# Kernel optimization log

Hardware: AMD Instinct MI355X
Metric: run time of the kernel (lower is better)

The kernel has to match this reference:

```python
import jax, jax.numpy as jnp
import numpy as np

HID = 4096
NH = 64
HD = HID // NH            # 64
ROT = int(0.5 * HD)       # 32, partial rotary
THETA = 25000.0
EPS = 1e-5
NEG = jnp.finfo(jnp.float32).min


def setup_inputs() -> dict:
    key = jax.random.key(0)
    ks = jax.random.split(key, 8)
    B, S = 1, 2048
    hidden_states = jax.random.normal(ks[0], (B, S, HID), dtype=jnp.float32)
    # causal additive mask [B,1,S,S]
    causal = jnp.where(jnp.tril(jnp.ones((S, S), dtype=bool)), 0.0, NEG)
    attention_mask = jnp.broadcast_to(causal, (B, 1, S, S)).astype(jnp.float32)
    position_ids = jnp.broadcast_to(jnp.arange(S, dtype=jnp.int32), (B, S))
    sc = 1.0 / np.sqrt(HID)
    W_qkv = jax.random.normal(ks[1], (HID, 3 * HID), dtype=jnp.float32) * sc
    b_qkv = jnp.zeros((3 * HID,), dtype=jnp.float32)
    W_dense = jax.random.normal(ks[2], (HID, HID), dtype=jnp.float32) * sc
    b_dense = jnp.zeros((HID,), dtype=jnp.float32)
    q_ln_w = jnp.ones((HD,), dtype=jnp.float32)
    q_ln_b = jnp.zeros((HD,), dtype=jnp.float32)
    k_ln_w = jnp.ones((HD,), dtype=jnp.float32)
    k_ln_b = jnp.zeros((HD,), dtype=jnp.float32)
    return dict(hidden_states=hidden_states, attention_mask=attention_mask,
                position_ids=position_ids, W_qkv=W_qkv, b_qkv=b_qkv,
                W_dense=W_dense, b_dense=b_dense,
                q_ln_w=q_ln_w, q_ln_b=q_ln_b, k_ln_w=k_ln_w, k_ln_b=k_ln_b)


def _layernorm(x, w, b):
    mu = jnp.mean(x, axis=-1, keepdims=True)
    var = jnp.mean(jnp.square(x - mu), axis=-1, keepdims=True)
    return (x - mu) * jax.lax.rsqrt(var + EPS) * w + b


def _rope_cos_sin(seq_len, position_ids):
    inv_freq = 1.0 / (THETA ** (jnp.arange(0, ROT, 2, dtype=jnp.float32) / ROT))
    t = jnp.arange(seq_len, dtype=jnp.float32)
    freqs = jnp.einsum('s,f->sf', t, inv_freq)        # [S, ROT/2]
    emb = jnp.concatenate([freqs, freqs], axis=-1)    # [S, ROT]
    cos = jnp.cos(emb)[position_ids][:, None, :, :]   # [B,1,S,ROT]
    sin = jnp.sin(emb)[position_ids][:, None, :, :]
    return cos, sin


def _rotate_half(x):
    x1, x2 = jnp.split(x, 2, axis=-1)
    return jnp.concatenate([-x2, x1], axis=-1)


def reference(hidden_states, attention_mask, position_ids, W_qkv, b_qkv,
              W_dense, b_dense, q_ln_w, q_ln_b, k_ln_w, k_ln_b):
    B, S, _ = hidden_states.shape
    fused = hidden_states @ W_qkv + b_qkv                 # [B,S,3*HID]
    fused = fused.reshape(B, S, NH, 3, HD)
    q, k, v = fused[..., 0, :], fused[..., 1, :], fused[..., 2, :]  # [B,S,NH,HD]
    q = _layernorm(q, q_ln_w, q_ln_b)
    k = _layernorm(k, k_ln_w, k_ln_b)
    q = q.transpose(0, 2, 1, 3)                           # [B,NH,S,HD]
    k = k.transpose(0, 2, 1, 3)
    v = v.transpose(0, 2, 1, 3)
    cos, sin = _rope_cos_sin(S, position_ids)
    q_rot, q_pass = q[..., :ROT], q[..., ROT:]
    k_rot, k_pass = k[..., :ROT], k[..., ROT:]
    q_rot = q_rot * cos + _rotate_half(q_rot) * sin
    k_rot = k_rot * cos + _rotate_half(k_rot) * sin
    q = jnp.concatenate([q_rot, q_pass], axis=-1)
    k = jnp.concatenate([k_rot, k_pass], axis=-1)
    scores = jnp.einsum('bhqd,bhkd->bhqk', q, k) / np.sqrt(HD)
    scores = scores + attention_mask
    probs = jax.nn.softmax(scores.astype(jnp.float32), axis=-1).astype(q.dtype)
    attn = jnp.einsum('bhqk,bhkd->bhqd', probs, v)        # [B,NH,S,HD]
    attn = attn.transpose(0, 2, 1, 3).reshape(B, S, HID)
    return attn @ W_dense + b_dense
```

## Files before the change

### kernel.cpp

```cpp
#include <hip/hip_runtime.h>
#include <hip/hip_bf16.h>


typedef __attribute__((ext_vector_type(4))) unsigned int u32x4;
typedef __attribute__((ext_vector_type(8))) __bf16 bf16x8;
typedef __attribute__((ext_vector_type(4))) float f32x4;

__device__ __forceinline__ bf16x8 frag_ld(const __hip_bfloat16* p) {
  return __builtin_bit_cast(bf16x8, *(const u32x4*)p);
}

__device__ __forceinline__ void gll16(const __hip_bfloat16* g,
                                      __hip_bfloat16* l) {
  __builtin_amdgcn_global_load_lds(
      (const __attribute__((address_space(1))) unsigned int*)g,
      (__attribute__((address_space(3))) unsigned int*)l, 16, 0, 0);
}

__global__ __launch_bounds__(256) void cvt_kernel(
    const float* __restrict__ in, __hip_bfloat16* __restrict__ out, int n4) {
  int i = blockIdx.x * 256 + threadIdx.x;
  if (i < n4) {
    float4 v = ((const float4*)in)[i];
    union { __hip_bfloat16 h[4]; unsigned long long u; } pk;
    pk.h[0] = __float2bfloat16(v.x);
    pk.h[1] = __float2bfloat16(v.y);
    pk.h[2] = __float2bfloat16(v.z);
    pk.h[3] = __float2bfloat16(v.w);
    ((unsigned long long*)out)[i] = pk.u;
  }
}

__global__ __launch_bounds__(256) void transpose_kernel(
    const float* __restrict__ W, __hip_bfloat16* __restrict__ WT,
    int K, int ldW, int colStride, int colOff) {
  __shared__ __align__(16) __hip_bfloat16 tile[64 * 72];
  const int t = threadIdx.x;
  const int c0 = blockIdx.x * colStride + colOff;
  const int n0 = blockIdx.x * 64;
  const int k0 = blockIdx.y * 64;
  for (int c = t; c < 1024; c += 256) {
    int row = c >> 4, col4 = (c & 15) << 2;
    float4 v = *(const float4*)&W[(size_t)(k0 + row) * ldW + c0 + col4];
    union { __hip_bfloat16 h[4]; unsigned long long u; } pk;
    pk.h[0] = __float2bfloat16(v.x);
    pk.h[1] = __float2bfloat16(v.y);
    pk.h[2] = __float2bfloat16(v.z);
    pk.h[3] = __float2bfloat16(v.w);
    *(unsigned long long*)&tile[row * 72 + col4] = pk.u;
  }
  __syncthreads();
  for (int c = t; c < 512; c += 256) {
    int row = c >> 3, col8 = (c & 7) << 3;
    union { __hip_bfloat16 h[8]; u32x4 v; } pk;
#pragma unroll
    for (int j = 0; j < 8; ++j) pk.h[j] = tile[(col8 + j) * 72 + row];
    *(u32x4*)&WT[(size_t)(n0 + row) * K + k0 + col8] = pk.v;
  }
}

__global__ __launch_bounds__(512, 2) void gemm256_kernel(
    const __hip_bfloat16* __restrict__ A, const __hip_bfloat16* __restrict__ BT,
    const float* __restrict__ bias, float* __restrict__ Cf,
    __hip_bfloat16* __restrict__ Cb, int M, int N, int K, int mode) {
  __shared__ __align__(16) __hip_bfloat16 As[3][128 * 64];
  __shared__ __align__(16) __hip_bfloat16 Bs[3][256 * 64];
  const int t = threadIdx.x;
  const int wv = t >> 6, lane = t & 63;
  const int qd = lane >> 4, md = lane & 15;
  const int wr = wv >> 2, wc = wv & 3;
  const int bid = blockIdx.x;
  const int swz = (bid & 7) * 32 + (bid >> 3);
  const int m0 = (swz >> 4) * 128, n0 = (swz & 15) * 256;
  const int rA = t >> 3;
  const int cg = (t & 7) ^ (rA & 7);
  const __hip_bfloat16* pA0 = A + (size_t)(m0 + rA) * K + cg * 8;
  const __hip_bfloat16* pA1 = A + (size_t)(m0 + 64 + rA) * K + cg * 8;
  const __hip_bfloat16* pB0 = BT + (size_t)(n0 + rA) * K + cg * 8;
  const __hip_bfloat16* pB1 = BT + (size_t)(n0 + 64 + rA) * K + cg * 8;
  const __hip_bfloat16* pB2 = BT + (size_t)(n0 + 128 + rA) * K + cg * 8;
  const __hip_bfloat16* pB3 = BT + (size_t)(n0 + 192 + rA) * K + cg * 8;
  const int ldsW = wv * 8 * 64;
  const int aRow = (wr * 64 + md) * 64;
  const int bRow = (wc * 64 + md) * 64;
  const int sw0 = (qd ^ (md & 7)) << 3;
  const int sw1 = ((4 + qd) ^ (md & 7)) << 3;
  f32x4 acc[4][4] = {};

  gll16(pA0, &As[0][ldsW]);
  gll16(pA1, &As[0][64 * 64 + ldsW]);
  gll16(pB0, &Bs[0][ldsW]);
  gll16(pB1, &Bs[0][64 * 64 + ldsW]);
  gll16(pB2, &Bs[0][128 * 64 + ldsW]);
  gll16(pB3, &Bs[0][192 * 64 + ldsW]);
  gll16(pA0 + 64, &As[1][ldsW]);
  gll16(pA1 + 64, &As[1][64 * 64 + ldsW]);
  gll16(pB0 + 64, &Bs[1][ldsW]);
  gll16(pB1 + 64, &Bs[1][64 * 64 + ldsW]);
  gll16(pB2 + 64, &Bs[1][128 * 64 + ldsW]);
  gll16(pB3 + 64, &Bs[1][192 * 64 + ldsW]);
  asm volatile("s_waitcnt vmcnt(6)" ::: "memory");
  __builtin_amdgcn_s_barrier();

  int cur = 0, nb = 2;
  for (int kt = 0; kt < 64; ++kt) {
    const __hip_bfloat16* Ac = As[cur];
    const __hip_bfloat16* Bc = Bs[cur];
    const bool st = kt < 62;
    const int koff = (kt + 2) * 64;
    bf16x8 af[4], bf[4];
#pragma unroll
    for (int i = 0; i < 4; ++i) af[i] = frag_ld(&Ac[aRow + i * 1024 + sw0]);
#pragma unroll
    for (int i = 0; i < 4; ++i) bf[i] = frag_ld(&Bc[bRow + i * 1024 + sw0]);
    if (st) {
      gll16(pA0 + koff, &As[nb][ldsW]);
      gll16(pA1 + koff, &As[nb][64 * 64 + ldsW]);
      gll16(pB0 + koff, &Bs[nb][ldsW]);
    }
    __builtin_amdgcn_s_barrier();
    asm volatile("s_waitcnt lgkmcnt(0)" ::: "memory");
    __builtin_amdgcn_s_setprio(1);
#pragma unroll
    for (int mi = 0; mi < 4; ++mi)
#pragma unroll
      for (int ni = 0; ni < 4; ++ni)
        acc[mi][ni] = __builtin_amdgcn_mfma_f32_16x16x32_bf16(
            af[mi], bf[ni], acc[mi][ni], 0, 0, 0);
    __builtin_amdgcn_s_setprio(0);
    __builtin_amdgcn_s_barrier();
#pragma unroll
    for (int i = 0; i < 4; ++i) af[i] = frag_ld(&Ac[aRow + i * 1024 + sw1]);
#pragma unroll
    for (int i = 0; i < 4; ++i) bf[i] = frag_ld(&Bc[bRow + i * 1024 + sw1]);
    if (st) {
      gll16(pB1 + koff, &Bs[nb][64 * 64 + ldsW]);
      gll16(pB2 + koff, &Bs[nb][128 * 64 + ldsW]);
      gll16(pB3 + koff, &Bs[nb][192 * 64 + ldsW]);
    }
    __builtin_amdgcn_s_barrier();
    asm volatile("s_waitcnt lgkmcnt(0)" ::: "memory");
    __builtin_amdgcn_s_setprio(1);
#pragma unroll
    for (int mi = 0; mi < 4; ++mi)
#pragma unroll
      for (int ni = 0; ni < 4; ++ni)
        acc[mi][ni] = __builtin_amdgcn_mfma_f32_16x16x32_bf16(
            af[mi], bf[ni], acc[mi][ni], 0, 0, 0);
    __builtin_amdgcn_s_setprio(0);
    if (kt < 62)
      asm volatile("s_waitcnt vmcnt(6)" ::: "memory");
    else if (kt < 63)
      asm volatile("s_waitcnt vmcnt(0)" ::: "memory");
    __builtin_amdgcn_s_barrier();
    cur = (cur == 2) ? 0 : cur + 1;
    nb = (nb == 2) ? 0 : nb + 1;
  }
#pragma unroll
  for (int ni = 0; ni < 4; ++ni) {
    int col = n0 + wc * 64 + ni * 16 + md;
    float bv = (mode == 0) ? bias[col] : bias[(col >> 6) * 192 + (col & 63)];
#pragma unroll
    for (int mi = 0; mi < 4; ++mi) {
      int rb = m0 + wr * 64 + mi * 16 + qd * 4;
#pragma unroll
      for (int r = 0; r < 4; ++r) {
        float v = acc[mi][ni][r] + bv;
        if (mode == 0)
          Cf[(size_t)(rb + r) * N + col] = v;
        else
          Cb[((size_t)(col >> 6) * M + rb + r) * 64 + (col & 63)] =
              __float2bfloat16(v);
      }
    }
  }
}

__device__ __forceinline__ float wred_sum(float v) {
#pragma unroll
  for (int x = 1; x < 64; x <<= 1) v += __shfl_xor(v, x, 64);
  return v;
}

__global__ __launch_bounds__(256) void lnrope_kernel(
    __hip_bfloat16* __restrict__ Q, __hip_bfloat16* __restrict__ K,
    const __hip_bfloat16* __restrict__ V, __hip_bfloat16* __restrict__ VT,
    const int* __restrict__ pos_ids,
    const float* __restrict__ qw, const float* __restrict__ qb,
    const float* __restrict__ kw, const float* __restrict__ kbias) {
  const int h = blockIdx.x;
  const int s0 = blockIdx.y * 64;
  const int t = threadIdx.x, wv = t >> 6, lane = t & 63;
  const float gq = qw[lane], bqv = qb[lane];
  const float gk = kw[lane], bkv = kbias[lane];
  const float invf = powf(25000.0f, -(float)(lane & 15) / 16.0f);
  for (int i = 0; i < 16; ++i) {
    int s = s0 + wv * 16 + i;
    size_t idx = ((size_t)h * 2048 + s) * 64 + lane;
    float q = (float)Q[idx];
    float k = (float)K[idx];
    float muq = wred_sum(q) * (1.0f / 64.0f);
    float dq = q - muq;
    float vq = wred_sum(dq * dq) * (1.0f / 64.0f);
    float qn = dq * rsqrtf(vq + 1e-5f) * gq + bqv;
    float muk = wred_sum(k) * (1.0f / 64.0f);
    float dk = k - muk;
    float vk = wred_sum(dk * dk) * (1.0f / 64.0f);
    float kn = dk * rsqrtf(vk + 1e-5f) * gk + bkv;
    float ang = (float)pos_ids[s] * invf;
    float sn, cs;
    sincosf(ang, &sn, &cs);
    float qo = __shfl_xor(qn, 16, 64);
    float ko = __shfl_xor(kn, 16, 64);
    float qr = qn, kr = kn;
    if (lane < 16) {
      qr = qn * cs - qo * sn; kr = kn * cs - ko * sn;
    } else if (lane < 32) {
      qr = qn * cs + qo * sn; kr = kn * cs + ko * sn;
    }
    Q[idx] = __float2bfloat16(qr * 0.18033688f);
    K[idx] = __float2bfloat16(kr);
  }
  __shared__ __align__(16) __hip_bfloat16 vt[64 * 72];
  for (int c = t; c < 512; c += 256) {
    int r = c >> 3, col8 = (c & 7) << 3;
    *(u32x4*)&vt[r * 72 + col8] =
        *(const u32x4*)&V[((size_t)h * 2048 + s0 + r) * 64 + col8];
  }
  __syncthreads();
  for (int c = t; c < 512; c += 256) {
    int d = c >> 3, col8 = (c & 7) << 3;
    union { __hip_bfloat16 hh[8]; u32x4 v; } pk;
#pragma unroll
    for (int j = 0; j < 8; ++j) pk.hh[j] = vt[(col8 + j) * 72 + d];
    *(u32x4*)&VT[((size_t)h * 64 + d) * 2048 + s0 + col8] = pk.v;
  }
}

__global__ __launch_bounds__(256) void fattn_kernel(
    const __hip_bfloat16* __restrict__ Q, const __hip_bfloat16* __restrict__ K,
    const __hip_bfloat16* __restrict__ VT, __hip_bfloat16* __restrict__ attn) {
  const int h = blockIdx.x, qb = 31 - blockIdx.y;
  const int t = threadIdx.x, wv = t >> 6, lane = t & 63;
  const int qd = lane >> 4, md = lane & 15;
  __shared__ __align__(16) __hip_bfloat16 Kls[64 * 72];
  __shared__ __align__(16) __hip_bfloat16 Vls[64 * 72];
  __shared__ __align__(16) __hip_bfloat16 Pls[64 * 72];
  const int q0 = qb * 64;
  const __hip_bfloat16* Qp = Q + ((size_t)h * 2048 + q0 + wv * 16 + md) * 64;
  bf16x8 qf0 = frag_ld(Qp + qd * 8);
  bf16x8 qf1 = frag_ld(Qp + 32 + qd * 8);
  float lp[4] = {0.f, 0.f, 0.f, 0.f};
  f32x4 O[4] = {};
  for (int kb = 0; kb <= qb; ++kb) {
    __syncthreads();
    for (int c = t; c < 512; c += 256) {
      int row = c >> 3, col8 = (c & 7) << 3;
      *(u32x4*)&Kls[row * 72 + col8] =
          *(const u32x4*)&K[((size_t)h * 2048 + kb * 64 + row) * 64 + col8];
      *(u32x4*)&Vls[row * 72 + col8] =
          *(const u32x4*)&VT[((size_t)h * 64 + row) * 2048 + kb * 64 + col8];
    }
    __syncthreads();
    const bool diag = (kb == qb);
    float pv[4][4];
#pragma unroll
    for (int nt = 0; nt < 4; ++nt) {
      f32x4 s4 = {};
      bf16x8 kf0 = frag_ld(&Kls[(nt * 16 + md) * 72 + qd * 8]);
      bf16x8 kf1 = frag_ld(&Kls[(nt * 16 + md) * 72 + 32 + qd * 8]);
      s4 = __builtin_amdgcn_mfma_f32_16x16x32_bf16(qf0, kf0, s4, 0, 0, 0);
      s4 = __builtin_amdgcn_mfma_f32_16x16x32_bf16(qf1, kf1, s4, 0, 0, 0);
      int key = nt * 16 + md;
#pragma unroll
      for (int r = 0; r < 4; ++r) {
        float p = exp2f(s4[r]);
        if (diag) p = (key > wv * 16 + qd * 4 + r) ? 0.f : p;
        pv[nt][r] = p;
        lp[r] += p;
      }
    }
#pragma unroll
    for (int nt = 0; nt < 4; ++nt)
#pragma unroll
      for (int r = 0; r < 4; ++r)
        Pls[(wv * 16 + qd * 4 + r) * 72 + nt * 16 + md] =
            __float2bfloat16(pv[nt][r]);
    bf16x8 pf0 = frag_ld(&Pls[(wv * 16 + md) * 72 + qd * 8]);
    bf16x8 pf1 = frag_ld(&Pls[(wv * 16 + md) * 72 + 32 + qd * 8]);
#pragma unroll
    for (int nt = 0; nt < 4; ++nt) {
      bf16x8 vf0 = frag_ld(&Vls[(nt * 16 + md) * 72 + qd * 8]);
      bf16x8 vf1 = frag_ld(&Vls[(nt * 16 + md) * 72 + 32 + qd * 8]);
      O[nt] = __builtin_amdgcn_mfma_f32_16x16x32_bf16(pf0, vf0, O[nt], 0, 0, 0);
      O[nt] = __builtin_amdgcn_mfma_f32_16x16x32_bf16(pf1, vf1, O[nt], 0, 0, 0);
    }
  }
#pragma unroll
  for (int r = 0; r < 4; ++r) {
#pragma unroll
    for (int x = 1; x < 16; x <<= 1) lp[r] += __shfl_xor(lp[r], x, 16);
    lp[r] = 1.0f / lp[r];
  }
#pragma unroll
  for (int nt = 0; nt < 4; ++nt) {
    int col = h * 64 + nt * 16 + md;
#pragma unroll
    for (int r = 0; r < 4; ++r) {
      int row = q0 + wv * 16 + qd * 4 + r;
      attn[(size_t)row * 4096 + col] = __float2bfloat16(O[nt][r] * lp[r]);
    }
  }
}

extern "C" void kernel_launch(void* const* d_in, const int* in_sizes, int n_in,
                              void* d_out, int out_size, void* d_ws,
                              size_t ws_size, hipStream_t stream) {
  const float* hidden = (const float*)d_in[0];
  const int* pos = (const int*)d_in[2];
  const float* Wqkv = (const float*)d_in[3];
  const float* bqkv = (const float*)d_in[4];
  const float* Wd = (const float*)d_in[5];
  const float* bd = (const float*)d_in[6];
  const float* qlw = (const float*)d_in[7];
  const float* qlb = (const float*)d_in[8];
  const float* klw = (const float*)d_in[9];
  const float* klb = (const float*)d_in[10];

  char* ws = (char*)d_ws;
  __hip_bfloat16* WpT = (__hip_bfloat16*)ws;
  __hip_bfloat16* VT = (__hip_bfloat16*)ws;
  __hip_bfloat16* attn = (__hip_bfloat16*)(ws + 16777216);
  __hip_bfloat16* Hb = (__hip_bfloat16*)(ws + 33554432);
  __hip_bfloat16* Qb = (__hip_bfloat16*)(ws + 50331648);
  __hip_bfloat16* Kb = (__hip_bfloat16*)(ws + 67108864);
  __hip_bfloat16* Vb = (__hip_bfloat16*)(ws + 83886080);
  __hip_bfloat16* WdT = (__hip_bfloat16*)(ws + 33554432);
  float* out = (float*)d_out;

  cvt_kernel<<<8192, 256, 0, stream>>>(hidden, Hb, 2097152);
  __hip_bfloat16* qkv_dst[3] = {Qb, Kb, Vb};
  for (int p = 0; p < 3; ++p) {
    transpose_kernel<<<dim3(64, 64), 256, 0, stream>>>(Wqkv, WpT, 4096, 12288,
                                                       192, p * 64);
    gemm256_kernel<<<256, 512, 0, stream>>>(Hb, WpT, bqkv + p * 64, nullptr,
                                            qkv_dst[p], 2048, 4096, 4096, 1);
  }
  lnrope_kernel<<<dim3(64, 32), 256, 0, stream>>>(Qb, Kb, Vb, VT, pos, qlw, qlb,
                                                  klw, klb);
  fattn_kernel<<<dim3(64, 32), 256, 0, stream>>>(Qb, Kb, VT, attn);
  transpose_kernel<<<dim3(64, 64), 256, 0, stream>>>(Wd, WdT, 4096, 4096, 64, 0);
  gemm256_kernel<<<256, 512, 0, stream>>>(attn, WdT, bd, out, nullptr,
                                          2048, 4096, 4096, 0);
}
```

Measured before the change: 785.3 us.

## Double-buffer K/V tiles in flash attention with async global-to-LDS loads

Replaces the synchronous register-staged K/V tile loads in the attention kernel with global_load_lds direct copies into double-buffered LDS, prefetching the next key block while the current one is computed. The padded layout becomes an XOR-swizzled unpadded layout to avoid bank conflicts, and s_setprio raises wave priority around the MFMA section. The pipeline depends on manual vmcnt waits and raw s_barrier, so ordering mistakes could race.

```diff
diff --git a/kernel.cpp b/kernel.cpp
--- a/kernel.cpp
+++ b/kernel.cpp
@@ -243,8 +243,8 @@
   const int h = blockIdx.x, qb = 31 - blockIdx.y;
   const int t = threadIdx.x, wv = t >> 6, lane = t & 63;
   const int qd = lane >> 4, md = lane & 15;
-  __shared__ __align__(16) __hip_bfloat16 Kls[64 * 72];
-  __shared__ __align__(16) __hip_bfloat16 Vls[64 * 72];
+  __shared__ __align__(16) __hip_bfloat16 Kls[2][64 * 64];
+  __shared__ __align__(16) __hip_bfloat16 Vls[2][64 * 64];
   __shared__ __align__(16) __hip_bfloat16 Pls[64 * 72];
   const int q0 = qb * 64;
   const __hip_bfloat16* Qp = Q + ((size_t)h * 2048 + q0 + wv * 16 + md) * 64;
@@ -252,23 +252,45 @@
   bf16x8 qf1 = frag_ld(Qp + 32 + qd * 8);
   float lp[4] = {0.f, 0.f, 0.f, 0.f};
   f32x4 O[4] = {};
+  const int srow = t >> 3;
+  const int scg = ((t & 7) ^ (srow & 7)) << 3;
+  const __hip_bfloat16* Kg = K + (size_t)h * 2048 * 64;
+  const __hip_bfloat16* Vg = VT + (size_t)h * 64 * 2048;
+  const int ldsW = wv * 512;
+  const int ksw0 = (qd ^ (md & 7)) << 3;
+  const int ksw1 = ((4 + qd) ^ (md & 7)) << 3;
+  {
+    int kb = 0;
+    gll16(Kg + (size_t)(kb * 64 + srow) * 64 + scg, &Kls[0][ldsW]);
+    gll16(Kg + (size_t)(kb * 64 + 32 + srow) * 64 + scg, &Kls[0][2048 + ldsW]);
+    gll16(Vg + (size_t)srow * 2048 + kb * 64 + scg, &Vls[0][ldsW]);
+    gll16(Vg + (size_t)(32 + srow) * 2048 + kb * 64 + scg, &Vls[0][2048 + ldsW]);
+  }
+  int cur = 0;
   for (int kb = 0; kb <= qb; ++kb) {
-    __syncthreads();
-    for (int c = t; c < 512; c += 256) {
-      int row = c >> 3, col8 = (c & 7) << 3;
-      *(u32x4*)&Kls[row * 72 + col8] =
-          *(const u32x4*)&K[((size_t)h * 2048 + kb * 64 + row) * 64 + col8];
-      *(u32x4*)&Vls[row * 72 + col8] =
-          *(const u32x4*)&VT[((size_t)h * 64 + row) * 2048 + kb * 64 + col8];
-    }
-    __syncthreads();
+    if (kb < qb) {
+      int nb = cur ^ 1, k1 = kb + 1;
+      gll16(Kg + (size_t)(k1 * 64 + srow) * 64 + scg, &Kls[nb][ldsW]);
+      gll16(Kg + (size_t)(k1 * 64 + 32 + srow) * 64 + scg,
+            &Kls[nb][2048 + ldsW]);
+      gll16(Vg + (size_t)srow * 2048 + k1 * 64 + scg, &Vls[nb][ldsW]);
+      gll16(Vg + (size_t)(32 + srow) * 2048 + k1 * 64 + scg,
+            &Vls[nb][2048 + ldsW]);
+      asm volatile("s_waitcnt vmcnt(4)" ::: "memory");
+    } else {
+      asm volatile("s_waitcnt vmcnt(0)" ::: "memory");
+    }
+    __builtin_amdgcn_s_barrier();
+    const __hip_bfloat16* Kc = Kls[cur];
+    const __hip_bfloat16* Vc = Vls[cur];
     const bool diag = (kb == qb);
     float pv[4][4];
+    __builtin_amdgcn_s_setprio(1);
 #pragma unroll
     for (int nt = 0; nt < 4; ++nt) {
       f32x4 s4 = {};
-      bf16x8 kf0 = frag_ld(&Kls[(nt * 16 + md) * 72 + qd * 8]);
-      bf16x8 kf1 = frag_ld(&Kls[(nt * 16 + md) * 72 + 32 + qd * 8]);
+      bf16x8 kf0 = frag_ld(&Kc[(nt * 16 + md) * 64 + ksw0]);
+      bf16x8 kf1 = frag_ld(&Kc[(nt * 16 + md) * 64 + ksw1]);
       s4 = __builtin_amdgcn_mfma_f32_16x16x32_bf16(qf0, kf0, s4, 0, 0, 0);
       s4 = __builtin_amdgcn_mfma_f32_16x16x32_bf16(qf1, kf1, s4, 0, 0, 0);
       int key = nt * 16 + md;
@@ -290,11 +312,14 @@
     bf16x8 pf1 = frag_ld(&Pls[(wv * 16 + md) * 72 + 32 + qd * 8]);
 #pragma unroll
     for (int nt = 0; nt < 4; ++nt) {
-      bf16x8 vf0 = frag_ld(&Vls[(nt * 16 + md) * 72 + qd * 8]);
-      bf16x8 vf1 = frag_ld(&Vls[(nt * 16 + md) * 72 + 32 + qd * 8]);
+      bf16x8 vf0 = frag_ld(&Vc[(nt * 16 + md) * 64 + ksw0]);
+      bf16x8 vf1 = frag_ld(&Vc[(nt * 16 + md) * 64 + ksw1]);
       O[nt] = __builtin_amdgcn_mfma_f32_16x16x32_bf16(pf0, vf0, O[nt], 0, 0, 0);
       O[nt] = __builtin_amdgcn_mfma_f32_16x16x32_bf16(pf1, vf1, O[nt], 0, 0, 0);
     }
+    __builtin_amdgcn_s_setprio(0);
+    __builtin_amdgcn_s_barrier();
+    cur ^= 1;
   }
 #pragma unroll
   for (int r = 0; r < 4; ++r) {
```

After: 802.6 us. 2.2% more time.

## Switch GEMM inner loop to 32x32x16 MFMA with adjusted LDS swizzle

Applied to the files above, without the earlier changes.

Replaces the 16x16x32 bf16 MFMA tiles with 32x32x16 MFMA tiles in the projection GEMM. Each wave now holds a 2x2 grid of 32x32 accumulators instead of 4x4 of 16x16. The LDS swizzle gains an extra XOR bit so the 32-row fragment reads avoid bank conflicts. The epilogue row mapping is updated to match. The goal is fewer MFMA issues and fewer LDS fragment reads per k-step, at the cost of a changed register layout and different output store patterns.

```diff
diff --git a/kernel.cpp b/kernel.cpp
--- a/kernel.cpp
+++ b/kernel.cpp
@@ -5,6 +5,7 @@
 typedef __attribute__((ext_vector_type(4))) unsigned int u32x4;
 typedef __attribute__((ext_vector_type(8))) __bf16 bf16x8;
 typedef __attribute__((ext_vector_type(4))) float f32x4;
+typedef __attribute__((ext_vector_type(16))) float f32x16;
 
 __device__ __forceinline__ bf16x8 frag_ld(const __hip_bfloat16* p) {
   return __builtin_bit_cast(bf16x8, *(const u32x4*)p);
@@ -67,25 +68,24 @@
   __shared__ __align__(16) __hip_bfloat16 Bs[3][256 * 64];
   const int t = threadIdx.x;
   const int wv = t >> 6, lane = t & 63;
-  const int qd = lane >> 4, md = lane & 15;
+  const int rl = lane & 31, eh = lane >> 5;
   const int wr = wv >> 2, wc = wv & 3;
   const int bid = blockIdx.x;
   const int swz = (bid & 7) * 32 + (bid >> 3);
   const int m0 = (swz >> 4) * 128, n0 = (swz & 15) * 256;
   const int rA = t >> 3;
-  const int cg = (t & 7) ^ (rA & 7);
+  const int cg = (t & 7) ^ (rA & 7) ^ (((rA >> 3) & 1) << 2);
   const __hip_bfloat16* pA0 = A + (size_t)(m0 + rA) * K + cg * 8;
   const __hip_bfloat16* pA1 = A + (size_t)(m0 + 64 + rA) * K + cg * 8;
   const __hip_bfloat16* pB0 = BT + (size_t)(n0 + rA) * K + cg * 8;
   const __hip_bfloat16* pB1 = BT + (size_t)(n0 + 64 + rA) * K + cg * 8;
   const __hip_bfloat16* pB2 = BT + (size_t)(n0 + 128 + rA) * K + cg * 8;
   const __hip_bfloat16* pB3 = BT + (size_t)(n0 + 192 + rA) * K + cg * 8;
-  const int ldsW = wv * 8 * 64;
-  const int aRow = (wr * 64 + md) * 64;
-  const int bRow = (wc * 64 + md) * 64;
-  const int sw0 = (qd ^ (md & 7)) << 3;
-  const int sw1 = ((4 + qd) ^ (md & 7)) << 3;
-  f32x4 acc[4][4] = {};
+  const int ldsW = wv * 512;
+  const int xr = (rl & 7) ^ (((rl >> 3) & 1) << 2);
+  const int aRow = (wr * 64 + rl) * 64;
+  const int bRow = (wc * 64 + rl) * 64;
+  f32x16 acc[2][2] = {};
 
   gll16(pA0, &As[0][ldsW]);
   gll16(pA1, &As[0][64 * 64 + ldsW]);
@@ -108,11 +108,17 @@
     const __hip_bfloat16* Bc = Bs[cur];
     const bool st = kt < 62;
     const int koff = (kt + 2) * 64;
-    bf16x8 af[4], bf[4];
-#pragma unroll
-    for (int i = 0; i < 4; ++i) af[i] = frag_ld(&Ac[aRow + i * 1024 + sw0]);
-#pragma unroll
-    for (int i = 0; i < 4; ++i) bf[i] = frag_ld(&Bc[bRow + i * 1024 + sw0]);
+    bf16x8 af[2][2], bf[2][2];
+#pragma unroll
+    for (int mi = 0; mi < 2; ++mi)
+#pragma unroll
+      for (int s = 0; s < 2; ++s)
+        af[mi][s] = frag_ld(&Ac[aRow + mi * 2048 + (((s * 2 + eh) ^ xr) << 3)]);
+#pragma unroll
+    for (int ni = 0; ni < 2; ++ni)
+#pragma unroll
+      for (int s = 0; s < 2; ++s)
+        bf[ni][s] = frag_ld(&Bc[bRow + ni * 2048 + (((s * 2 + eh) ^ xr) << 3)]);
     if (st) {
       gll16(pA0 + koff, &As[nb][ldsW]);
       gll16(pA1 + koff, &As[nb][64 * 64 + ldsW]);
@@ -122,17 +128,27 @@
     asm volatile("s_waitcnt lgkmcnt(0)" ::: "memory");
     __builtin_amdgcn_s_setprio(1);
 #pragma unroll
-    for (int mi = 0; mi < 4; ++mi)
-#pragma unroll
-      for (int ni = 0; ni < 4; ++ni)
-        acc[mi][ni] = __builtin_amdgcn_mfma_f32_16x16x32_bf16(
-            af[mi], bf[ni], acc[mi][ni], 0, 0, 0);
+    for (int mi = 0; mi < 2; ++mi)
+#pragma unroll
+      for (int ni = 0; ni < 2; ++ni)
+#pragma unroll
+        for (int s = 0; s < 2; ++s)
+          acc[mi][ni] = __builtin_amdgcn_mfma_f32_32x32x16_bf16(
+              af[mi][s], bf[ni][s], acc[mi][ni], 0, 0, 0);
     __builtin_amdgcn_s_setprio(0);
     __builtin_amdgcn_s_barrier();
 #pragma unroll
-    for (int i = 0; i < 4; ++i) af[i] = frag_ld(&Ac[aRow + i * 1024 + sw1]);
-#pragma unroll
-    for (int i = 0; i < 4; ++i) bf[i] = frag_ld(&Bc[bRow + i * 1024 + sw1]);
+    for (int mi = 0; mi < 2; ++mi)
+#pragma unroll
+      for (int s = 0; s < 2; ++s)
+        af[mi][s] =
+            frag_ld(&Ac[aRow + mi * 2048 + (((4 + s * 2 + eh) ^ xr) << 3)]);
+#pragma unroll
+    for (int ni = 0; ni < 2; ++ni)
+#pragma unroll
+      for (int s = 0; s < 2; ++s)
+        bf[ni][s] =
+            frag_ld(&Bc[bRow + ni * 2048 + (((4 + s * 2 + eh) ^ xr) << 3)]);
     if (st) {
       gll16(pB1 + koff, &Bs[nb][64 * 64 + ldsW]);
       gll16(pB2 + koff, &Bs[nb][128 * 64 + ldsW]);
@@ -142,11 +158,13 @@
     asm volatile("s_waitcnt lgkmcnt(0)" ::: "memory");
     __builtin_amdgcn_s_setprio(1);
 #pragma unroll
-    for (int mi = 0; mi < 4; ++mi)
-#pragma unroll
-      for (int ni = 0; ni < 4; ++ni)
-        acc[mi][ni] = __builtin_amdgcn_mfma_f32_16x16x32_bf16(
-            af[mi], bf[ni], acc[mi][ni], 0, 0, 0);
+    for (int mi = 0; mi < 2; ++mi)
+#pragma unroll
+      for (int ni = 0; ni < 2; ++ni)
+#pragma unroll
+        for (int s = 0; s < 2; ++s)
+          acc[mi][ni] = __builtin_amdgcn_mfma_f32_32x32x16_bf16(
+              af[mi][s], bf[ni][s], acc[mi][ni], 0, 0, 0);
     __builtin_amdgcn_s_setprio(0);
     if (kt < 62)
       asm volatile("s_waitcnt vmcnt(6)" ::: "memory");
@@ -157,19 +175,20 @@
     nb = (nb == 2) ? 0 : nb + 1;
   }
 #pragma unroll
-  for (int ni = 0; ni < 4; ++ni) {
-    int col = n0 + wc * 64 + ni * 16 + md;
+  for (int ni = 0; ni < 2; ++ni) {
+    int col = n0 + wc * 64 + ni * 32 + rl;
     float bv = (mode == 0) ? bias[col] : bias[(col >> 6) * 192 + (col & 63)];
 #pragma unroll
-    for (int mi = 0; mi < 4; ++mi) {
-      int rb = m0 + wr * 64 + mi * 16 + qd * 4;
-#pragma unroll
-      for (int r = 0; r < 4; ++r) {
-        float v = acc[mi][ni][r] + bv;
+    for (int mi = 0; mi < 2; ++mi) {
+      int rbase = m0 + wr * 64 + mi * 32 + 4 * eh;
+#pragma unroll
+      for (int reg = 0; reg < 16; ++reg) {
+        int row = rbase + (reg & 3) + 8 * (reg >> 2);
+        float v = acc[mi][ni][reg] + bv;
         if (mode == 0)
-          Cf[(size_t)(rb + r) * N + col] = v;
+          Cf[(size_t)row * N + col] = v;
         else
-          Cb[((size_t)(col >> 6) * M + rb + r) * 64 + (col & 63)] =
+          Cb[((size_t)(col >> 6) * M + row) * 64 + (col & 63)] =
               __float2bfloat16(v);
       }
     }
```

Measured after the change: 819.3 us. +4.3%, slower.

## Fuse q/k layernorm and rotary embedding into QKV GEMM epilogue

Applied to the files above, without the earlier changes.

Moves the per-head LayerNorm and partial RoPE for Q and K into the QKV GEMM epilogue, using 16-lane shuffles since each wave column covers exactly one head. The separate lnrope kernel is reduced to a V transpose only. This removes a full read/write pass over Q and K and one launch, at the cost of a heavier GEMM epilogue with possible register pressure.

```diff
diff --git a/kernel.cpp b/kernel.cpp
--- a/kernel.cpp
+++ b/kernel.cpp
@@ -62,7 +62,9 @@
 __global__ __launch_bounds__(512, 2) void gemm256_kernel(
     const __hip_bfloat16* __restrict__ A, const __hip_bfloat16* __restrict__ BT,
     const float* __restrict__ bias, float* __restrict__ Cf,
-    __hip_bfloat16* __restrict__ Cb, int M, int N, int K, int mode) {
+    __hip_bfloat16* __restrict__ Cb, const float* __restrict__ lnw,
+    const float* __restrict__ lnb, const int* __restrict__ pos,
+    int M, int N, int K, int mode) {
   __shared__ __align__(16) __hip_bfloat16 As[3][128 * 64];
   __shared__ __align__(16) __hip_bfloat16 Bs[3][256 * 64];
   const int t = threadIdx.x;
@@ -156,71 +158,77 @@
     cur = (cur == 2) ? 0 : cur + 1;
     nb = (nb == 2) ? 0 : nb + 1;
   }
-#pragma unroll
-  for (int ni = 0; ni < 4; ++ni) {
-    int col = n0 + wc * 64 + ni * 16 + md;
-    float bv = (mode == 0) ? bias[col] : bias[(col >> 6) * 192 + (col & 63)];
+  if (mode == 0) {
+#pragma unroll
+    for (int ni = 0; ni < 4; ++ni) {
+      int col = n0 + wc * 64 + ni * 16 + md;
+      float bv = bias[col];
+#pragma unroll
+      for (int mi = 0; mi < 4; ++mi) {
+        int rb = m0 + wr * 64 + mi * 16 + qd * 4;
+#pragma unroll
+        for (int r = 0; r < 4; ++r)
+          Cf[(size_t)(rb + r) * N + col] = acc[mi][ni][r] + bv;
+      }
+    }
+  } else {
+    float g[4], bb[4], bv[4];
+    int hd[4];
+#pragma unroll
+    for (int ni = 0; ni < 4; ++ni) {
+      int col = n0 + wc * 64 + ni * 16 + md;
+      hd[ni] = col;
+      bv[ni] = bias[(col >> 6) * 192 + (col & 63)];
+      if (mode >= 2) { g[ni] = lnw[ni * 16 + md]; bb[ni] = lnb[ni * 16 + md]; }
+    }
+    const float invf =
+        (mode >= 2) ? powf(25000.0f, -(float)md / 16.0f) : 0.0f;
 #pragma unroll
     for (int mi = 0; mi < 4; ++mi) {
-      int rb = m0 + wr * 64 + mi * 16 + qd * 4;
 #pragma unroll
       for (int r = 0; r < 4; ++r) {
-        float v = acc[mi][ni][r] + bv;
-        if (mode == 0)
-          Cf[(size_t)(rb + r) * N + col] = v;
-        else
-          Cb[((size_t)(col >> 6) * M + rb + r) * 64 + (col & 63)] =
-              __float2bfloat16(v);
+        int row = m0 + wr * 64 + mi * 16 + qd * 4 + r;
+        float v[4];
+#pragma unroll
+        for (int ni = 0; ni < 4; ++ni) v[ni] = acc[mi][ni][r] + bv[ni];
+        if (mode >= 2) {
+          float s = v[0] + v[1] + v[2] + v[3];
+#pragma unroll
+          for (int x = 1; x < 16; x <<= 1) s += __shfl_xor(s, x, 16);
+          float mu = s * (1.0f / 64.0f);
+          float ss = 0.0f;
+#pragma unroll
+          for (int ni = 0; ni < 4; ++ni) {
+            v[ni] -= mu;
+            ss += v[ni] * v[ni];
+          }
+#pragma unroll
+          for (int x = 1; x < 16; x <<= 1) ss += __shfl_xor(ss, x, 16);
+          float rs = rsqrtf(ss * (1.0f / 64.0f) + 1e-5f);
+#pragma unroll
+          for (int ni = 0; ni < 4; ++ni) v[ni] = v[ni] * rs * g[ni] + bb[ni];
+          float sn, cs;
+          sincosf((float)pos[row] * invf, &sn, &cs);
+          float v0 = v[0], v1 = v[1];
+          v[0] = v0 * cs - v1 * sn;
+          v[1] = v1 * cs + v0 * sn;
+          if (mode == 2) {
+#pragma unroll
+            for (int ni = 0; ni < 4; ++ni) v[ni] *= 0.18033688f;
+          }
+        }
+#pragma unroll
+        for (int ni = 0; ni < 4; ++ni)
+          Cb[((size_t)(hd[ni] >> 6) * M + row) * 64 + (hd[ni] & 63)] =
+              __float2bfloat16(v[ni]);
       }
     }
   }
 }
 
-__device__ __forceinline__ float wred_sum(float v) {
-#pragma unroll
-  for (int x = 1; x < 64; x <<= 1) v += __shfl_xor(v, x, 64);
-  return v;
-}
-
-__global__ __launch_bounds__(256) void lnrope_kernel(
-    __hip_bfloat16* __restrict__ Q, __hip_bfloat16* __restrict__ K,
-    const __hip_bfloat16* __restrict__ V, __hip_bfloat16* __restrict__ VT,
-    const int* __restrict__ pos_ids,
-    const float* __restrict__ qw, const float* __restrict__ qb,
-    const float* __restrict__ kw, const float* __restrict__ kbias) {
-  const int h = blockIdx.x;
-  const int s0 = blockIdx.y * 64;
-  const int t = threadIdx.x, wv = t >> 6, lane = t & 63;
-  const float gq = qw[lane], bqv = qb[lane];
-  const float gk = kw[lane], bkv = kbias[lane];
-  const float invf = powf(25000.0f, -(float)(lane & 15) / 16.0f);
-  for (int i = 0; i < 16; ++i) {
-    int s = s0 + wv * 16 + i;
-    size_t idx = ((size_t)h * 2048 + s) * 64 + lane;
-    float q = (float)Q[idx];
-    float k = (float)K[idx];
-    float muq = wred_sum(q) * (1.0f / 64.0f);
-    float dq = q - muq;
-    float vq = wred_sum(dq * dq) * (1.0f / 64.0f);
-    float qn = dq * rsqrtf(vq + 1e-5f) * gq + bqv;
-    float muk = wred_sum(k) * (1.0f / 64.0f);
-    float dk = k - muk;
-    float vk = wred_sum(dk * dk) * (1.0f / 64.0f);
-    float kn = dk * rsqrtf(vk + 1e-5f) * gk + bkv;
-    float ang = (float)pos_ids[s] * invf;
-    float sn, cs;
-    sincosf(ang, &sn, &cs);
-    float qo = __shfl_xor(qn, 16, 64);
-    float ko = __shfl_xor(kn, 16, 64);
-    float qr = qn, kr = kn;
-    if (lane < 16) {
-      qr = qn * cs - qo * sn; kr = kn * cs - ko * sn;
-    } else if (lane < 32) {
-      qr = qn * cs + qo * sn; kr = kn * cs + ko * sn;
-    }
-    Q[idx] = __float2bfloat16(qr * 0.18033688f);
-    K[idx] = __float2bfloat16(kr);
-  }
+__global__ __launch_bounds__(256) void vtrans_kernel(
+    const __hip_bfloat16* __restrict__ V, __hip_bfloat16* __restrict__ VT) {
+  const int h = blockIdx.x, s0 = blockIdx.y * 64, t = threadIdx.x;
   __shared__ __align__(16) __hip_bfloat16 vt[64 * 72];
   for (int c = t; c < 512; c += 256) {
     int r = c >> 3, col8 = (c & 7) << 3;
@@ -340,16 +348,20 @@
 
   cvt_kernel<<<8192, 256, 0, stream>>>(hidden, Hb, 2097152);
   __hip_bfloat16* qkv_dst[3] = {Qb, Kb, Vb};
+  const float* lnw_p[3] = {qlw, klw, nullptr};
+  const float* lnb_p[3] = {qlb, klb, nullptr};
+  const int mode_p[3] = {2, 3, 1};
   for (int p = 0; p < 3; ++p) {
     transpose_kernel<<<dim3(64, 64), 256, 0, stream>>>(Wqkv, WpT, 4096, 12288,
                                                        192, p * 64);
     gemm256_kernel<<<256, 512, 0, stream>>>(Hb, WpT, bqkv + p * 64, nullptr,
-                                            qkv_dst[p], 2048, 4096, 4096, 1);
-  }
-  lnrope_kernel<<<dim3(64, 32), 256, 0, stream>>>(Qb, Kb, Vb, VT, pos, qlw, qlb,
-                                                  klw, klb);
+                                            qkv_dst[p], lnw_p[p], lnb_p[p], pos,
+                                            2048, 4096, 4096, mode_p[p]);
+  }
+  vtrans_kernel<<<dim3(64, 32), 256, 0, stream>>>(Vb, VT);
   fattn_kernel<<<dim3(64, 32), 256, 0, stream>>>(Qb, Kb, VT, attn);
   transpose_kernel<<<dim3(64, 64), 256, 0, stream>>>(Wd, WdT, 4096, 4096, 64, 0);
-  gemm256_kernel<<<256, 512, 0, stream>>>(attn, WdT, bd, out, nullptr,
-                                          2048, 4096, 4096, 0);
-}
+  gemm256_kernel<<<256, 512, 0, stream>>>(attn, WdT, bd, out, nullptr, nullptr,
+                                          nullptr, nullptr, 2048, 4096, 4096,
+                                          0);
+}
```

Measured after the change: 762.6 us, median of 2. 1.03x faster.
